# Performance work log

Measured on AMD Instinct MI355X. Metric: run time of the kernel, lower is better.

## Reference

```python
import jax, jax.numpy as jnp
import numpy as np

D, H_DIM, HEADS = 512, 2048, 8

def rmsnorm(x, w):
    eps = jnp.finfo(x.dtype).eps
    return x * jax.lax.rsqrt(jnp.mean(x * x, axis=-1, keepdims=True) + eps) * w

def setup_inputs() -> dict:
    key = jax.random.key(0)
    ks = jax.random.split(key, 16)
    B, N = 2, 2048
    s_d = 1.0 / np.sqrt(D)
    s_h = 1.0 / np.sqrt(H_DIM)
    inp = {
        "x": jax.random.normal(ks[0], (B, N, D), jnp.float32),
        "DA": jax.random.randint(ks[1], (B, 1, N, N), 0, 2, jnp.int32),
        "Wq": jax.random.normal(ks[2], (D, D), jnp.float32) * s_d,
        "bq": jnp.zeros((D,), jnp.float32),
        "Wk": jax.random.normal(ks[3], (D, D), jnp.float32) * s_d,
        "bk": jnp.zeros((D,), jnp.float32),
        "Wv": jax.random.normal(ks[4], (D, D), jnp.float32) * s_d,
        "bv": jnp.zeros((D,), jnp.float32),
        "W1": jax.random.normal(ks[5], (H_DIM, D), jnp.float32) * s_d,
        "b1": jnp.zeros((H_DIM,), jnp.float32),
        "W2": jax.random.normal(ks[6], (H_DIM, D), jnp.float32) * s_d,
        "b2": jnp.zeros((H_DIM,), jnp.float32),
        "W3": jax.random.normal(ks[7], (D, H_DIM), jnp.float32) * s_h,
        "b3": jnp.zeros((D,), jnp.float32),
        "g1": jnp.ones((D,), jnp.float32),
        "g2": jnp.ones((D,), jnp.float32),
    }
    return inp

def reference(x, DA, Wq, bq, Wk, bk, Wv, bv, W1, b1, W2, b2, W3, b3, g1, g2):
    B, N, _ = x.shape
    hd = D // HEADS  # head_dim = 64
    xn = rmsnorm(x, g1)
    # projections (torch Linear: y = x @ W.T + b), split heads -> [B,H,N,hd]
    def split(t):
        return t.reshape(B, N, HEADS, hd).transpose(0, 2, 1, 3)
    q = split(xn @ Wq.T + bq)
    k = split(xn @ Wk.T + bk)
    v = split(xn @ Wv.T + bv)
    scores = jnp.einsum("bhnd,bhmd->bhnm", q, k) / np.sqrt(hd)
    scores = jnp.where(DA == 0, jnp.asarray(-1e20, scores.dtype), scores)
    attn = jax.nn.softmax(scores, axis=-1)
    o = jnp.einsum("bhnm,bhmd->bhnd", attn, v)
    o = o.transpose(0, 2, 1, 3).reshape(B, N, D)
    h = x + o
    hn = rmsnorm(h, g2)
    x2 = hn @ W1.T + b1
    x3 = hn @ W2.T + b2
    out = h + (jax.nn.silu(x2) * x3) @ W3.T + b3
    return out
```

## Files before the change

### kernel.cpp

```cpp
#include <hip/hip_runtime.h>

typedef unsigned short u16;
typedef unsigned int   u32;
typedef unsigned long long u64;

using bf16x8 = __attribute__((ext_vector_type(8))) __bf16;
using f32x4  = __attribute__((ext_vector_type(4))) float;
using us8    = __attribute__((ext_vector_type(8))) u16;
using us4v   = __attribute__((ext_vector_type(4))) u16;

#define NB_TOK   4096
#define DD       512
#define HDIM     2048
#define SEQ      2048
#define EPS_F32  1.1920929e-7f
#define SM_SHIFT2 23.083120654223414f
#define Q_SCALE   0.18033688011112042f

__device__ __forceinline__ u16 f32_to_bf16(float f) {
  u32 u = __float_as_uint(f);
  u += 0x7fffu + ((u >> 16) & 1u);
  return (u16)(u >> 16);
}
__device__ __forceinline__ float bf16_to_f32(u16 h) {
  return __uint_as_float(((u32)h) << 16);
}
__device__ __forceinline__ bf16x8 ld_frag(const u16* p) {
  return __builtin_bit_cast(bf16x8, *(const us8*)p);
}
__device__ __forceinline__ void gload_lds16(const void* g, void* l) {
  __builtin_amdgcn_global_load_lds(
      (__attribute__((address_space(1))) void*)(void*)g,
      (__attribute__((address_space(3))) void*)l, 16, 0, 0);
}

__global__ __launch_bounds__(256) void k_pre(
    const float* __restrict__ wq, const float* __restrict__ wk,
    const float* __restrict__ wv, const float* __restrict__ w1,
    const float* __restrict__ w2, const float* __restrict__ w3,
    const int* __restrict__ da, const float* __restrict__ x,
    const float* __restrict__ g1,
    u16* __restrict__ wqkv, u16* __restrict__ w1b,
    u16* __restrict__ w2b, u16* __restrict__ w3b,
    u64* __restrict__ maskT, u16* __restrict__ xn) {
  int bx = blockIdx.x;
  if (bx < 3840) {
    int e = (bx * 256 + threadIdx.x) * 4;
    const float* src; u16* dst; int off;
    if      (e <  262144) { src = wq; dst = wqkv;          off = e; }
    else if (e <  524288) { src = wk; dst = wqkv + 262144; off = e -  262144; }
    else if (e <  786432) { src = wv; dst = wqkv + 524288; off = e -  524288; }
    else if (e < 1835008) { src = w1; dst = w1b;           off = e -  786432; }
    else if (e < 2883584) { src = w2; dst = w2b;           off = e - 1835008; }
    else                  { src = w3; dst = w3b;           off = e - 2883584; }
    float4 v = *(const float4*)(src + off);
    us4v o;
    o[0] = f32_to_bf16(v.x); o[1] = f32_to_bf16(v.y);
    o[2] = f32_to_bf16(v.z); o[3] = f32_to_bf16(v.w);
    *(us4v*)(dst + off) = o;
  } else if (bx < 4864) {
    int lane = threadIdx.x & 63, wave = threadIdx.x >> 6;
    int row = (bx - 3840) * 4 + wave;
    int b = row >> 11, r = row & 2047;
    const int* src = da + (size_t)row * SEQ;
    #pragma unroll 4
    for (int w = 0; w < 32; ++w) {
      int d = src[w * 64 + lane];
      u64 bal = __ballot(d != 0);
      if (lane == 0) maskT[((size_t)(b * 32 + w)) * SEQ + r] = bal;
    }
  } else {
    int lane = threadIdx.x & 63, wave = threadIdx.x >> 6;
    int row = (bx - 4864) * 4 + wave;
    size_t base = (size_t)row * DD + lane * 8;
    float4 a = *(const float4*)(x + base);
    float4 b = *(const float4*)(x + base + 4);
    float ss = a.x*a.x + a.y*a.y + a.z*a.z + a.w*a.w
             + b.x*b.x + b.y*b.y + b.z*b.z + b.w*b.w;
    #pragma unroll
    for (int m = 1; m < 64; m <<= 1) ss += __shfl_xor(ss, m);
    float sc = rsqrtf(ss * (1.0f / DD) + EPS_F32);
    float4 ga = *(const float4*)(g1 + lane * 8);
    float4 gb = *(const float4*)(g1 + lane * 8 + 4);
    us8 o;
    o[0] = f32_to_bf16(a.x * sc * ga.x); o[1] = f32_to_bf16(a.y * sc * ga.y);
    o[2] = f32_to_bf16(a.z * sc * ga.z); o[3] = f32_to_bf16(a.w * sc * ga.w);
    o[4] = f32_to_bf16(b.x * sc * gb.x); o[5] = f32_to_bf16(b.y * sc * gb.y);
    o[6] = f32_to_bf16(b.z * sc * gb.z); o[7] = f32_to_bf16(b.w * sc * gb.w);
    *(us8*)(xn + base) = o;
  }
}

template <int NB>
__device__ __forceinline__ void gemm32(const u16* __restrict__ A,
                                       const u16* __restrict__ B0,
                                       const u16* __restrict__ B1,
                                       int K, int mblk, int nblk,
                                       int kbeg, int iters,
                                       u16* lA, u16* lB,
                                       f32x4 (*acc)[4][2]) {
  const int lane = threadIdx.x & 63, wave = threadIdx.x >> 6;
  const int l15 = lane & 15, quad = lane >> 4;
  const int wmt = (wave >> 1) * 4, wnt = (wave & 1) * 2;
  constexpr int CPW = 2 + NB;

  auto stage = [&](int buf, int k0) {
    #pragma unroll
    for (int i = 0; i < CPW; ++i) {
      int id = wave * CPW + i;
      if (id < 8) {
        gload_lds16(A + (size_t)(mblk + id * 16 + l15) * K + k0 + quad * 8,
                    lA + buf * 4096 + id * 512);
      } else {
        int id2 = id - 8, bi = id2 >> 2, nt = id2 & 3;
        const u16* B = bi ? B1 : B0;
        gload_lds16(B + (size_t)(nblk + nt * 16 + l15) * K + k0 + quad * 8,
                    lB + bi * 4096 + buf * 2048 + nt * 512);
      }
    }
  };

  stage(0, kbeg);
  __syncthreads();
  for (int it = 0; it < iters; ++it) {
    if (it + 1 < iters) stage((it + 1) & 1, kbeg + (it + 1) * 32);
    int buf = it & 1;
    bf16x8 af[4];
    #pragma unroll
    for (int mt = 0; mt < 4; ++mt)
      af[mt] = ld_frag(lA + buf * 4096 + (wmt + mt) * 512 + lane * 8);
    #pragma unroll
    for (int bi = 0; bi < NB; ++bi)
      #pragma unroll
      for (int nt = 0; nt < 2; ++nt) {
        bf16x8 b = ld_frag(lB + bi * 4096 + buf * 2048 + (wnt + nt) * 512 + lane * 8);
        #pragma unroll
        for (int mt = 0; mt < 4; ++mt)
          acc[bi][mt][nt] = __builtin_amdgcn_mfma_f32_16x16x32_bf16(
              af[mt], b, acc[bi][mt][nt], 0, 0, 0);
      }
    __syncthreads();
  }
}

__global__ __launch_bounds__(256, 4) void k_qkv(const u16* __restrict__ xn,
                                                const u16* __restrict__ wqkv,
                                                const float* __restrict__ bq,
                                                const float* __restrict__ bk,
                                                const float* __restrict__ bv,
                                                u16* __restrict__ qb,
                                                u16* __restrict__ kb,
                                                u16* __restrict__ vt) {
  __shared__ u16 lA[8192], lB[4096];
  int z = blockIdx.z;
  const u16* Bp = wqkv + z * (DD * DD);
  const float* bias = (z == 0) ? bq : ((z == 1) ? bk : bv);
  float scale = (z == 0) ? Q_SCALE : 1.0f;
  int mblk = blockIdx.x * 128, nblk = blockIdx.y * 64;
  f32x4 acc[1][4][2];
  #pragma unroll
  for (int mt = 0; mt < 4; ++mt)
    #pragma unroll
    for (int nt = 0; nt < 2; ++nt) acc[0][mt][nt] = (f32x4)0.0f;
  gemm32<1>(xn, Bp, nullptr, DD, mblk, nblk, 0, 16, lA, lB, acc);
  int lane = threadIdx.x & 63, wave = threadIdx.x >> 6;
  int l15 = lane & 15, quad = lane >> 4;
  int wm = (wave >> 1) * 64, wn = (wave & 1) * 32;
  if (z < 2) {
    u16* out = z ? kb : qb;
    #pragma unroll
    for (int mt = 0; mt < 4; ++mt)
      #pragma unroll
      for (int nt = 0; nt < 2; ++nt) {
        int n = nblk + wn + nt * 16 + l15;
        float bn = bias[n];
        #pragma unroll
        for (int r = 0; r < 4; ++r) {
          int m = mblk + wm + mt * 16 + quad * 4 + r;
          out[(size_t)m * DD + n] = f32_to_bf16((acc[0][mt][nt][r] + bn) * scale);
        }
      }
  } else {
    #pragma unroll
    for (int mt = 0; mt < 4; ++mt)
      #pragma unroll
      for (int nt = 0; nt < 2; ++nt) {
        int n = nblk + wn + nt * 16 + l15;
        float bn = bias[n];
        int m = mblk + wm + mt * 16 + quad * 4;
        int b = m >> 11, tok = m & 2047;
        us4v o;
        #pragma unroll
        for (int r = 0; r < 4; ++r) o[r] = f32_to_bf16(acc[0][mt][nt][r] + bn);
        *(us4v*)(vt + ((size_t)(b * 8 + (n >> 6)) * 64 + (n & 63)) * SEQ + tok) = o;
      }
  }
}

__global__ __launch_bounds__(256) void k_attn(const u16* __restrict__ q,
                                              const u16* __restrict__ k,
                                              const u16* __restrict__ vT,
                                              const u64* __restrict__ maskT,
                                              u16* __restrict__ Opart,
                                              float* __restrict__ lpart) {
  __shared__ u16 lK[8192], lV[8192], lP[4 * 32 * 72];
  int tid = threadIdx.x, lane = tid & 63, wave = tid >> 6;
  int l15 = lane & 15, quad = lane >> 4;
  int bh = blockIdx.y, b = bh >> 3, h = bh & 7;
  int q0 = blockIdx.x * 128;
  int z = blockIdx.z;
  int kvbase = z * 512;
  const u16* kg = k + (size_t)(b * SEQ + kvbase) * DD + h * 64;
  const u16* vg = vT + (size_t)bh * 64 * SEQ + kvbase;
  const u64* mg = maskT + ((size_t)(b * 32 + z * 8)) * SEQ + q0 + wave * 32 + l15;

  #pragma unroll
  for (int i = 0; i < 2; ++i) {
    int c = wave * 2 + i;
    int mt = c >> 1, ks = c & 1;
    gload_lds16(kg + (size_t)(mt * 16 + l15) * DD + ks * 32 + quad * 8, lK + c * 512);
    gload_lds16(vg + (size_t)(mt * 16 + l15) * SEQ + ks * 32 + quad * 8, lV + c * 512);
  }

  const u16* qrow = q + (size_t)(b * SEQ + q0 + wave * 32 + l15) * DD + h * 64;
  bf16x8 qa[2][2];
  #pragma unroll
  for (int nq = 0; nq < 2; ++nq)
    #pragma unroll
    for (int ks = 0; ks < 2; ++ks)
      qa[nq][ks] = ld_frag(qrow + (size_t)nq * 16 * DD + ks * 32 + quad * 8);
  __syncthreads();

  f32x4 oa[2][4];
  float ls[2] = {0.0f, 0.0f};
  #pragma unroll
  for (int mq = 0; mq < 2; ++mq)
    #pragma unroll
    for (int dt = 0; dt < 4; ++dt) oa[mq][dt] = (f32x4)0.0f;

  u16* pw = lP + wave * 2304;

  for (int t = 0; t < 8; ++t) {
    const u16* lKc = lK + (t & 1) * 4096;
    const u16* lVc = lV + (t & 1) * 4096;

    u64 mw[2];
    #pragma unroll
    for (int nq = 0; nq < 2; ++nq)
      mw[nq] = mg[(size_t)t * SEQ + nq * 16] >> (quad * 4);

    if (t + 1 < 8) {
      int kv1 = (t + 1) * 64;
      u16* dK = lK + ((t + 1) & 1) * 4096;
      u16* dV = lV + ((t + 1) & 1) * 4096;
      #pragma unroll
      for (int i = 0; i < 2; ++i) {
        int c = wave * 2 + i;
        int mt = c >> 1, ks = c & 1;
        gload_lds16(kg + (size_t)(kv1 + mt * 16 + l15) * DD + ks * 32 + quad * 8, dK + c * 512);
        gload_lds16(vg + (size_t)(mt * 16 + l15) * SEQ + kv1 + ks * 32 + quad * 8, dV + c * 512);
      }
    }

    f32x4 sa[2][4];
    #pragma unroll
    for (int nq = 0; nq < 2; ++nq)
      #pragma unroll
      for (int mt = 0; mt < 4; ++mt) sa[nq][mt] = (f32x4)0.0f;
    #pragma unroll
    for (int ks = 0; ks < 2; ++ks) {
      bf16x8 ka[4];
      #pragma unroll
      for (int mt = 0; mt < 4; ++mt)
        ka[mt] = ld_frag(lKc + mt * 1024 + ks * 512 + lane * 8);
      #pragma unroll
      for (int nq = 0; nq < 2; ++nq)
        #pragma unroll
        for (int mt = 0; mt < 4; ++mt)
          sa[nq][mt] = __builtin_amdgcn_mfma_f32_16x16x32_bf16(
              ka[mt], qa[nq][ks], sa[nq][mt], 0, 0, 0);
    }

    #pragma unroll
    for (int nq = 0; nq < 2; ++nq)
      #pragma unroll
      for (int mt = 0; mt < 4; ++mt) {
        u32 nib = (u32)(mw[nq] >> (mt * 16)) & 0xFu;
        u32 pb[4];
        #pragma unroll
        for (int r = 0; r < 4; ++r) {
          float p = __builtin_amdgcn_exp2f(sa[nq][mt][r] - SM_SHIFT2);
          p = (nib >> r) & 1u ? p : 0.0f;
          u32 ub = __float_as_uint(p) & 0xffff0000u;
          ls[nq] += __uint_as_float(ub);
          pb[r] = ub;
        }
        u32 lo = __builtin_amdgcn_perm(pb[1], pb[0], 0x07060302u);
        u32 hi = __builtin_amdgcn_perm(pb[3], pb[2], 0x07060302u);
        u64 pk = ((u64)hi << 32) | lo;
        *(u64*)(pw + (nq * 16 + l15) * 72 + mt * 16 + quad * 4) = pk;
      }

    #pragma unroll
    for (int ks = 0; ks < 2; ++ks) {
      bf16x8 pa[2], vb[4];
      #pragma unroll
      for (int mq = 0; mq < 2; ++mq)
        pa[mq] = ld_frag(pw + (mq * 16 + l15) * 72 + ks * 32 + quad * 8);
      #pragma unroll
      for (int dt = 0; dt < 4; ++dt)
        vb[dt] = ld_frag(lVc + dt * 1024 + ks * 512 + lane * 8);
      #pragma unroll
      for (int mq = 0; mq < 2; ++mq)
        #pragma unroll
        for (int dt = 0; dt < 4; ++dt)
          oa[mq][dt] = __builtin_amdgcn_mfma_f32_16x16x32_bf16(
              pa[mq], vb[dt], oa[mq][dt], 0, 0, 0);
    }

    __syncthreads();
  }

  #pragma unroll
  for (int nq = 0; nq < 2; ++nq) {
    ls[nq] += __shfl_xor(ls[nq], 16);
    ls[nq] += __shfl_xor(ls[nq], 32);
    if (quad == 0)
      lpart[((size_t)z * 16 + bh) * SEQ + q0 + wave * 32 + nq * 16 + l15] = ls[nq];
  }

  u16* Og = Opart + (size_t)z * NB_TOK * DD;
  #pragma unroll
  for (int mq = 0; mq < 2; ++mq)
    #pragma unroll
    for (int r = 0; r < 4; ++r) {
      int m = q0 + wave * 32 + mq * 16 + quad * 4 + r;
      u16* dst = Og + (size_t)(b * SEQ + m) * DD + h * 64;
      #pragma unroll
      for (int dt = 0; dt < 4; ++dt)
        dst[dt * 16 + l15] = f32_to_bf16(oa[mq][dt][r]);
    }
}

__global__ __launch_bounds__(256) void k_rms2(const float* __restrict__ x,
                                              const u16* __restrict__ Opart,
                                              const float* __restrict__ lpart,
                                              const float* __restrict__ b3,
                                              const float* __restrict__ g2,
                                              float* __restrict__ outinit,
                                              u16* __restrict__ hn) {
  int lane = threadIdx.x & 63, wave = threadIdx.x >> 6;
  int row = blockIdx.x * 4 + wave;
  int b = row >> 11, tok = row & 2047, hh = lane >> 3;
  size_t base = (size_t)row * DD + lane * 8;
  float lsum = 0.0f;
  #pragma unroll
  for (int z = 0; z < 4; ++z)
    lsum += lpart[((size_t)(z * 16 + b * 8 + hh)) * SEQ + tok];
  float inv = (lsum > 0.0f) ? (1.0f / lsum) : 0.0f;
  float ov[8] = {0,0,0,0,0,0,0,0};
  #pragma unroll
  for (int z = 0; z < 4; ++z) {
    us8 o = *(const us8*)(Opart + (size_t)z * NB_TOK * DD + base);
    #pragma unroll
    for (int j = 0; j < 8; ++j) ov[j] += bf16_to_f32(o[j]);
  }
  float4 a = *(const float4*)(x + base);
  float4 bb = *(const float4*)(x + base + 4);
  float hv[8];
  hv[0] = a.x  + ov[0] * inv; hv[1] = a.y  + ov[1] * inv;
  hv[2] = a.z  + ov[2] * inv; hv[3] = a.w  + ov[3] * inv;
  hv[4] = bb.x + ov[4] * inv; hv[5] = bb.y + ov[5] * inv;
  hv[6] = bb.z + ov[6] * inv; hv[7] = bb.w + ov[7] * inv;
  float ss = 0.0f;
  #pragma unroll
  for (int j = 0; j < 8; ++j) ss += hv[j] * hv[j];
  #pragma unroll
  for (int m = 1; m < 64; m <<= 1) ss += __shfl_xor(ss, m);
  float sc = rsqrtf(ss * (1.0f / DD) + EPS_F32);
  float4 c0 = *(const float4*)(b3 + lane * 8);
  float4 c1 = *(const float4*)(b3 + lane * 8 + 4);
  float4 w0 = {hv[0] + c0.x, hv[1] + c0.y, hv[2] + c0.z, hv[3] + c0.w};
  float4 w1 = {hv[4] + c1.x, hv[5] + c1.y, hv[6] + c1.z, hv[7] + c1.w};
  *(float4*)(outinit + base) = w0;
  *(float4*)(outinit + base + 4) = w1;
  float4 ga = *(const float4*)(g2 + lane * 8);
  float4 gb = *(const float4*)(g2 + lane * 8 + 4);
  us8 hb;
  hb[0] = f32_to_bf16(hv[0] * sc * ga.x); hb[1] = f32_to_bf16(hv[1] * sc * ga.y);
  hb[2] = f32_to_bf16(hv[2] * sc * ga.z); hb[3] = f32_to_bf16(hv[3] * sc * ga.w);
  hb[4] = f32_to_bf16(hv[4] * sc * gb.x); hb[5] = f32_to_bf16(hv[5] * sc * gb.y);
  hb[6] = f32_to_bf16(hv[6] * sc * gb.z); hb[7] = f32_to_bf16(hv[7] * sc * gb.w);
  *(us8*)(hn + base) = hb;
}

__global__ __launch_bounds__(256, 4) void k_ffn12(const u16* __restrict__ hn,
                                                  const u16* __restrict__ w1,
                                                  const u16* __restrict__ w2,
                                                  const float* __restrict__ b1,
                                                  const float* __restrict__ b2,
                                                  u16* __restrict__ g) {
  __shared__ u16 lA[8192], lB[8192];
  int mblk = blockIdx.x * 128, nblk = blockIdx.y * 64;
  f32x4 acc[2][4][2];
  #pragma unroll
  for (int bi = 0; bi < 2; ++bi)
    #pragma unroll
    for (int mt = 0; mt < 4; ++mt)
      #pragma unroll
      for (int nt = 0; nt < 2; ++nt) acc[bi][mt][nt] = (f32x4)0.0f;
  gemm32<2>(hn, w1, w2, DD, mblk, nblk, 0, 16, lA, lB, acc);
  int lane = threadIdx.x & 63, wave = threadIdx.x >> 6;
  int l15 = lane & 15, quad = lane >> 4;
  int wm = (wave >> 1) * 64, wn = (wave & 1) * 32;
  #pragma unroll
  for (int mt = 0; mt < 4; ++mt)
    #pragma unroll
    for (int nt = 0; nt < 2; ++nt) {
      int n = nblk + wn + nt * 16 + l15;
      float bb1 = b1[n], bb2 = b2[n];
      #pragma unroll
      for (int r = 0; r < 4; ++r) {
        int m = mblk + wm + mt * 16 + quad * 4 + r;
        float x2 = acc[0][mt][nt][r] + bb1;
        float x3 = acc[1][mt][nt][r] + bb2;
        float si = x2 / (1.0f + __expf(-x2));
        g[(size_t)m * HDIM + n] = f32_to_bf16(si * x3);
      }
    }
}

__global__ __launch_bounds__(256, 4) void k_ffn3(const u16* __restrict__ g,
                                                 const u16* __restrict__ w3,
                                                 float* __restrict__ out) {
  __shared__ u16 lA[8192], lB[4096];
  int mblk = blockIdx.x * 128, nblk = blockIdx.y * 64, z = blockIdx.z;
  f32x4 acc[1][4][2];
  #pragma unroll
  for (int mt = 0; mt < 4; ++mt)
    #pragma unroll
    for (int nt = 0; nt < 2; ++nt) acc[0][mt][nt] = (f32x4)0.0f;
  gemm32<1>(g, w3, nullptr, HDIM, mblk, nblk, z * 512, 16, lA, lB, acc);
  int lane = threadIdx.x & 63, wave = threadIdx.x >> 6;
  int l15 = lane & 15, quad = lane >> 4;
  int wm = (wave >> 1) * 64, wn = (wave & 1) * 32;
  #pragma unroll
  for (int mt = 0; mt < 4; ++mt)
    #pragma unroll
    for (int nt = 0; nt < 2; ++nt) {
      int n = nblk + wn + nt * 16 + l15;
      #pragma unroll
      for (int r = 0; r < 4; ++r) {
        int m = mblk + wm + mt * 16 + quad * 4 + r;
        atomicAdd(out + (size_t)m * DD + n, acc[0][mt][nt][r]);
      }
    }
}

#define MB(x) ((size_t)(x) * 1048576)
#define WS_XN    MB(0)
#define WS_WQKV  MB(4)
#define WS_W1B   MB(6)
#define WS_W2B   MB(8)
#define WS_W3B   MB(10)
#define WS_MASK  MB(12)
#define WS_QB    MB(16)
#define WS_KB    MB(20)
#define WS_VT    MB(24)
#define WS_OP    MB(28)
#define WS_LP    MB(44)
#define WS_HN    MB(45)
#define WS_G     MB(49)

extern "C" void kernel_launch(void* const* d_in, const int* in_sizes, int n_in,
                              void* d_out, int out_size, void* d_ws, size_t ws_size,
                              hipStream_t stream) {
  (void)in_sizes; (void)n_in; (void)out_size; (void)ws_size;
  const float* x  = (const float*)d_in[0];
  const int*   DA = (const int*)d_in[1];
  const float* Wq = (const float*)d_in[2];
  const float* bq = (const float*)d_in[3];
  const float* Wk = (const float*)d_in[4];
  const float* bk = (const float*)d_in[5];
  const float* Wv = (const float*)d_in[6];
  const float* bv = (const float*)d_in[7];
  const float* W1 = (const float*)d_in[8];
  const float* b1 = (const float*)d_in[9];
  const float* W2 = (const float*)d_in[10];
  const float* b2 = (const float*)d_in[11];
  const float* W3 = (const float*)d_in[12];
  const float* b3 = (const float*)d_in[13];
  const float* g1 = (const float*)d_in[14];
  const float* g2 = (const float*)d_in[15];
  float* out = (float*)d_out;
  char* w = (char*)d_ws;

  u16* xn   = (u16*)(w + WS_XN);
  u16* wqkv = (u16*)(w + WS_WQKV);
  u16* w1b  = (u16*)(w + WS_W1B);
  u16* w2b  = (u16*)(w + WS_W2B);
  u16* w3b  = (u16*)(w + WS_W3B);
  u64* mskT = (u64*)(w + WS_MASK);
  u16* qb   = (u16*)(w + WS_QB);
  u16* kb   = (u16*)(w + WS_KB);
  u16* vt   = (u16*)(w + WS_VT);
  u16* Op   = (u16*)(w + WS_OP);
  float* lp = (float*)(w + WS_LP);
  u16* hn   = (u16*)(w + WS_HN);
  u16* gb   = (u16*)(w + WS_G);

  k_pre<<<5888, 256, 0, stream>>>(Wq, Wk, Wv, W1, W2, W3, DA, x, g1,
                                  wqkv, w1b, w2b, w3b, mskT, xn);
  k_qkv<<<dim3(32, 8, 3), 256, 0, stream>>>(xn, wqkv, bq, bk, bv, qb, kb, vt);
  k_attn<<<dim3(16, 16, 4), 256, 0, stream>>>(qb, kb, vt, mskT, Op, lp);
  k_rms2<<<1024, 256, 0, stream>>>(x, Op, lp, b3, g2, out, hn);
  k_ffn12<<<dim3(32, 32), 256, 0, stream>>>(hn, w1b, w2b, b1, b2, gb);
  k_ffn3<<<dim3(32, 8, 4), 256, 0, stream>>>(gb, w3b, out);
}
```

Measured before the change: 280.6 us.

## Compute softmax row sums via MFMA with ones and drop split-K in FFN3

The attention kernel stops accumulating the softmax denominator with scalar adds and cross-lane shuffles. It instead runs an extra MFMA of the P tile against a vector of bf16 ones, so the row sums come straight out of the matrix unit and use the same rounded P values as the PV product. The FFN down-projection stops splitting K four ways with float atomics and runs the full K loop per block, writing with a plain read-add-store. This removes atomic traffic but cuts the grid for that kernel to a quarter, which lowers parallelism.

```diff
diff --git a/kernel.cpp b/kernel.cpp
--- a/kernel.cpp
+++ b/kernel.cpp
@@ -231,12 +231,18 @@
       qa[nq][ks] = ld_frag(qrow + (size_t)nq * 16 * DD + ks * 32 + quad * 8);
   __syncthreads();
 
-  f32x4 oa[2][4];
-  float ls[2] = {0.0f, 0.0f};
-  #pragma unroll
-  for (int mq = 0; mq < 2; ++mq)
+  us8 ones_u;
+  #pragma unroll
+  for (int j = 0; j < 8; ++j) ones_u[j] = 0x3f80;
+  const bf16x8 ones = __builtin_bit_cast(bf16x8, ones_u);
+
+  f32x4 oa[2][4], oal[2];
+  #pragma unroll
+  for (int mq = 0; mq < 2; ++mq) {
+    oal[mq] = (f32x4)0.0f;
     #pragma unroll
     for (int dt = 0; dt < 4; ++dt) oa[mq][dt] = (f32x4)0.0f;
+  }
 
   u16* pw = lP + wave * 2304;
 
@@ -291,9 +297,7 @@
         for (int r = 0; r < 4; ++r) {
           float p = __builtin_amdgcn_exp2f(sa[nq][mt][r] - SM_SHIFT2);
           p = (nib >> r) & 1u ? p : 0.0f;
-          u32 ub = __float_as_uint(p) & 0xffff0000u;
-          ls[nq] += __uint_as_float(ub);
-          pb[r] = ub;
+          pb[r] = __float_as_uint(p);
         }
         u32 lo = __builtin_amdgcn_perm(pb[1], pb[0], 0x07060302u);
         u32 hi = __builtin_amdgcn_perm(pb[3], pb[2], 0x07060302u);
@@ -311,22 +315,26 @@
       for (int dt = 0; dt < 4; ++dt)
         vb[dt] = ld_frag(lVc + dt * 1024 + ks * 512 + lane * 8);
       #pragma unroll
-      for (int mq = 0; mq < 2; ++mq)
+      for (int mq = 0; mq < 2; ++mq) {
         #pragma unroll
         for (int dt = 0; dt < 4; ++dt)
           oa[mq][dt] = __builtin_amdgcn_mfma_f32_16x16x32_bf16(
               pa[mq], vb[dt], oa[mq][dt], 0, 0, 0);
+        oal[mq] = __builtin_amdgcn_mfma_f32_16x16x32_bf16(
+            pa[mq], ones, oal[mq], 0, 0, 0);
+      }
     }
 
     __syncthreads();
   }
 
-  #pragma unroll
-  for (int nq = 0; nq < 2; ++nq) {
-    ls[nq] += __shfl_xor(ls[nq], 16);
-    ls[nq] += __shfl_xor(ls[nq], 32);
-    if (quad == 0)
-      lpart[((size_t)z * 16 + bh) * SEQ + q0 + wave * 32 + nq * 16 + l15] = ls[nq];
+  if (l15 == 0) {
+    #pragma unroll
+    for (int mq = 0; mq < 2; ++mq)
+      #pragma unroll
+      for (int r = 0; r < 4; ++r)
+        lpart[((size_t)z * 16 + bh) * SEQ + q0 + wave * 32 + mq * 16 + quad * 4 + r] =
+            oal[mq][r];
   }
 
   u16* Og = Opart + (size_t)z * NB_TOK * DD;
@@ -434,13 +442,13 @@
                                                  const u16* __restrict__ w3,
                                                  float* __restrict__ out) {
   __shared__ u16 lA[8192], lB[4096];
-  int mblk = blockIdx.x * 128, nblk = blockIdx.y * 64, z = blockIdx.z;
+  int mblk = blockIdx.x * 128, nblk = blockIdx.y * 64;
   f32x4 acc[1][4][2];
   #pragma unroll
   for (int mt = 0; mt < 4; ++mt)
     #pragma unroll
     for (int nt = 0; nt < 2; ++nt) acc[0][mt][nt] = (f32x4)0.0f;
-  gemm32<1>(g, w3, nullptr, HDIM, mblk, nblk, z * 512, 16, lA, lB, acc);
+  gemm32<1>(g, w3, nullptr, HDIM, mblk, nblk, 0, 64, lA, lB, acc);
   int lane = threadIdx.x & 63, wave = threadIdx.x >> 6;
   int l15 = lane & 15, quad = lane >> 4;
   int wm = (wave >> 1) * 64, wn = (wave & 1) * 32;
@@ -452,7 +460,8 @@
       #pragma unroll
       for (int r = 0; r < 4; ++r) {
         int m = mblk + wm + mt * 16 + quad * 4 + r;
-        atomicAdd(out + (size_t)m * DD + n, acc[0][mt][nt][r]);
+        size_t idx = (size_t)m * DD + n;
+        out[idx] = out[idx] + acc[0][mt][nt][r];
       }
     }
 }
@@ -515,5 +524,5 @@
   k_attn<<<dim3(16, 16, 4), 256, 0, stream>>>(qb, kb, vt, mskT, Op, lp);
   k_rms2<<<1024, 256, 0, stream>>>(x, Op, lp, b3, g2, out, hn);
   k_ffn12<<<dim3(32, 32), 256, 0, stream>>>(hn, w1b, w2b, b1, b2, gb);
-  k_ffn3<<<dim3(32, 8, 4), 256, 0, stream>>>(gb, w3b, out);
-}
+  k_ffn3<<<dim3(32, 8), 256, 0, stream>>>(gb, w3b, out);
+}
```

Measured after the change: 272.9 us. 2.7% less time.
